# Performance work log

Hardware: AMD Instinct MI355X
Metric: run time of the kernel (lower is better)

Reference implementation:

```python
import jax, jax.numpy as jnp
import numpy as np

N_EMBD = 768
N_HEAD = 8
HEAD_DIM = N_EMBD // N_HEAD


def setup_inputs() -> dict:
    key = jax.random.key(0)
    k1, k2, k3, k4, k5 = jax.random.split(key, 5)
    B, T, C = 8, 1024, N_EMBD
    scale = 0.02
    return {
        "x": jax.random.normal(k1, (B, T, C), dtype=jnp.float32),
        "W_attn": jax.random.normal(k2, (C, 3 * C), dtype=jnp.float32) * scale,
        "b_attn": jnp.zeros((3 * C,), dtype=jnp.float32),
        "W_proj": jax.random.normal(k3, (C, C), dtype=jnp.float32) * scale,
        "b_proj": jnp.zeros((C,), dtype=jnp.float32),
    }


def reference(x, W_attn, b_attn, W_proj, b_proj):
    B, T, C = x.shape
    H, D = N_HEAD, HEAD_DIM
    qkv = x @ W_attn + b_attn                      # [B,T,3C]
    q, k, v = jnp.split(qkv, 3, axis=-1)
    # [B,H,T,D]
    q = q.reshape(B, T, H, D).transpose(0, 2, 1, 3)
    k = k.reshape(B, T, H, D).transpose(0, 2, 1, 3)
    v = v.reshape(B, T, H, D).transpose(0, 2, 1, 3)
    att = jnp.einsum("bhqd,bhkd->bhqk", q, k) * (1.0 / jnp.sqrt(jnp.float32(D)))
    causal = jnp.tril(jnp.ones((T, T), dtype=bool))
    att = jnp.where(causal[None, None], att, jnp.float32(-jnp.inf))
    att = jax.nn.softmax(att, axis=-1)
    y = jnp.einsum("bhqk,bhkd->bhqd", att, v)      # [B,H,T,D]
    y = y.transpose(0, 2, 1, 3).reshape(B, T, C)
    return y @ W_proj + b_proj
```

## Files before the change

kernel.cpp:

```cpp
#include <hip/hip_runtime.h>
#include <math.h>

#define B_ 8
#define T_ 1024
#define C_ 768
#define H_ 8
#define D_ 96
#define M_ (B_ * T_)
#define N1_ (3 * C_)
#define KD_ 768
#define QS_ 1536

typedef __bf16 bf16x8 __attribute__((ext_vector_type(8)));
typedef float f32x4 __attribute__((ext_vector_type(4)));
typedef float f32x16 __attribute__((ext_vector_type(16)));

__device__ __forceinline__ unsigned short f2bf(float f) {
  unsigned int u = __float_as_uint(f);
  u += 0x7FFF + ((u >> 16) & 1);
  return (unsigned short)(u >> 16);
}

__device__ __forceinline__ void load_lds16(const void* g, void* l) {
  __builtin_amdgcn_global_load_lds(
      (const __attribute__((address_space(1))) unsigned int*)g,
      (__attribute__((address_space(3))) unsigned int*)l, 16, 0, 0);
}

__global__ __launch_bounds__(256) void prep_kernel(
    const float* __restrict__ x, unsigned short* __restrict__ xb,
    const float* __restrict__ Wa, unsigned short* __restrict__ WaT,
    const float* __restrict__ Wp, unsigned short* __restrict__ WpT) {
  __shared__ float Lt[32][33];
  int bid = blockIdx.x;
  if (bid < 6144) {
    int i = (bid * 256 + threadIdx.x) * 4;
    float4 v = *(const float4*)(x + i);
    ushort4 o;
    o.x = f2bf(v.x); o.y = f2bf(v.y); o.z = f2bf(v.z); o.w = f2bf(v.w);
    *(ushort4*)(xb + i) = o;
    return;
  }
  bid -= 6144;
  const float* W; unsigned short* WT; int Nd;
  if (bid < 1728) { W = Wa; WT = WaT; Nd = N1_; }
  else            { W = Wp; WT = WpT; Nd = C_; bid -= 1728; }
  const int r0 = (bid % 24) * 32;
  const int c0 = (bid / 24) * 32;
#pragma unroll
  for (int i = 0; i < 4; ++i) {
    int e = threadIdx.x + 256 * i;
    int r = e >> 5, c = e & 31;
    Lt[r][c] = W[(size_t)(r0 + r) * Nd + c0 + c];
  }
  __syncthreads();
#pragma unroll
  for (int i = 0; i < 4; ++i) {
    int e = threadIdx.x + 256 * i;
    int rr = e >> 5, cc = e & 31;
    WT[(size_t)(c0 + rr) * KD_ + r0 + cc] = f2bf(Lt[cc][rr]);
  }
}

template <bool OUTF32, bool VSCAT>
__global__ __launch_bounds__(256, 4) void gemm_mfma_kernel(
    const unsigned short* __restrict__ A, const unsigned short* __restrict__ Bt,
    const float* __restrict__ bias, void* __restrict__ Cout,
    unsigned short* __restrict__ vt, int N,
    int sc_lim, float sc, int mmask, int mshift) {
  constexpr int NCH = 16;
  constexpr int CPW = 4;
  __shared__ __align__(16) unsigned short Sb[2][NCH * 512];
  const int tid = threadIdx.x;
  const int w = tid >> 6, l = tid & 63;
  const int l31 = l & 31, lh = l >> 5;
  const int bid = blockIdx.x;
  const int m0 = (bid & mmask) * 128, n0 = (bid >> mshift) * 128;
  const int wrb = (w >> 1) * 2;
  const int wnb = (w & 1) * 2;

  f32x16 acc[2][2];
#pragma unroll
  for (int i = 0; i < 2; ++i)
#pragma unroll
    for (int j = 0; j < 2; ++j)
#pragma unroll
      for (int r = 0; r < 16; ++r) acc[i][j][r] = 0.f;

  const unsigned short* gp[CPW];
#pragma unroll
  for (int i = 0; i < CPW; ++i) {
    const int c = w * CPW + i;
    const int rr = (c & 7) * 16 + (l >> 2);
    const int ck = 8 * ((l & 3) ^ ((l >> 4) & 3));
    gp[i] = (c < 8) ? A  + (size_t)(m0 + rr) * KD_ + ck
                    : Bt + (size_t)(n0 + rr) * KD_ + ck;
  }

#pragma unroll
  for (int i = 0; i < CPW; ++i) {
    load_lds16(gp[i], &Sb[0][(w * CPW + i) * 512]);
    gp[i] += 32;
  }
  asm volatile("s_waitcnt vmcnt(0)" ::: "memory");
  __builtin_amdgcn_s_barrier();
  asm volatile("" ::: "memory");

  const int rhi = l31 >> 4;
  const int rlo = (l31 & 15) * 32;
  const int rx  = (l31 >> 2) & 3;

  int cur = 0;
  for (int k0 = 0; k0 < KD_; k0 += 32) {
    const bool more = (k0 + 32 < KD_);
    if (more) {
#pragma unroll
      for (int i = 0; i < CPW; ++i) {
        load_lds16(gp[i], &Sb[cur ^ 1][(w * CPW + i) * 512]);
        gp[i] += 32;
      }
    }

#pragma unroll
    for (int kh = 0; kh < 2; ++kh) {
      const int q = 2 * kh + lh;
      bf16x8 af[2], bfr[2];
#pragma unroll
      for (int mi = 0; mi < 2; ++mi)
        af[mi] = *(const bf16x8*)
            &Sb[cur][((wrb + mi) * 2 + rhi) * 512 + rlo + ((q ^ rx)) * 8];
#pragma unroll
      for (int ni = 0; ni < 2; ++ni)
        bfr[ni] = *(const bf16x8*)
            &Sb[cur][(8 + (wnb + ni) * 2 + rhi) * 512 + rlo + ((q ^ rx)) * 8];
#pragma unroll
      for (int mi = 0; mi < 2; ++mi)
#pragma unroll
        for (int ni = 0; ni < 2; ++ni)
          acc[mi][ni] = __builtin_amdgcn_mfma_f32_32x32x16_bf16(
              af[mi], bfr[ni], acc[mi][ni], 0, 0, 0);
    }

    if (more) {
      asm volatile("s_waitcnt vmcnt(0)" ::: "memory");
      asm volatile("" ::: "memory");
      __builtin_amdgcn_s_barrier();
      asm volatile("" ::: "memory");
    }
    cur ^= 1;
  }

  const bool vblock = VSCAT && (n0 >= 1536);
#pragma unroll
  for (int mi = 0; mi < 2; ++mi) {
    const int rowb = m0 + (wrb + mi) * 32 + 4 * lh;
#pragma unroll
    for (int ni = 0; ni < 2; ++ni) {
      const int col = n0 + (wnb + ni) * 32 + l31;
      const float bv = bias[col];
      if (!vblock) {
        const float mul = (col < sc_lim) ? sc : 1.f;
#pragma unroll
        for (int r = 0; r < 16; ++r) {
          const int row = rowb + (r & 3) + 8 * (r >> 2);
          float v = (acc[mi][ni][r] + bv) * mul;
          if (OUTF32)
            ((float*)Cout)[(size_t)row * N + col] = v;
          else
            ((unsigned short*)Cout)[(size_t)row * N + col] = f2bf(v);
        }
      } else {
        const int x = col - 1536;
        const int h = x / 96, d = x % 96;
#pragma unroll
        for (int r = 0; r < 16; ++r) {
          const int row = rowb + (r & 3) + 8 * (r >> 2);
          const int bb = row >> 10, t = row & 1023;
          vt[((size_t)(bb * H_ + h) * D_ + d) * T_ + t] =
              f2bf(acc[mi][ni][r] + bv);
        }
      }
    }
  }
}

__global__ __launch_bounds__(256) void attn_mfma_kernel(
    const unsigned short* __restrict__ qkv,
    const unsigned short* __restrict__ vt,
    unsigned short* __restrict__ y) {
  __shared__ __align__(16) unsigned short KV[2][24 * 512];
  __shared__ __align__(16) unsigned short Pt[4][16][72];

  const int tid = threadIdx.x;
  const int w = tid >> 6, l = tid & 63;
  const int lm = l & 15, lq = l >> 4;
  const int bh = blockIdx.x & 63, pi = blockIdx.x >> 6;
  const int b = bh >> 3, h = bh & 7;
  const size_t bT = (size_t)b * T_;

  bf16x8 onef;
#pragma unroll
  for (int i = 0; i < 8; ++i) onef[i] = (__bf16)1.0f;

  auto issue = [&](int j0, int buf) {
#pragma unroll
    for (int i = 0; i < 6; ++i) {
      const int c = w * 6 + i;
      const unsigned short* g;
      if (c < 12) {
        const int kc = c >> 2, nb = c & 3;
        g = qkv + (bT + j0 + nb * 16 + lm) * QS_ + C_ + h * D_ + kc * 32 + lq * 8;
      } else {
        const int cv = c - 12;
        const int db = cv >> 1, vc = cv & 1;
        g = vt + ((size_t)bh * D_ + db * 16 + lm) * T_ + j0 + vc * 32 + lq * 8;
      }
      load_lds16(g, &KV[buf][c * 512]);
    }
  };

  int cur = 0;
  issue(0, 0);

  for (int half = 0; half < 2; ++half) {
    const int qt = half ? (15 - pi) : pi;
    const int q0 = qt * 64;

    bf16x8 qf[3];
    {
      const unsigned short* qp =
          qkv + (bT + q0 + w * 16 + lm) * QS_ + h * D_ + lq * 8;
      qf[0] = *(const bf16x8*)(qp);
      qf[1] = *(const bf16x8*)(qp + 32);
      qf[2] = *(const bf16x8*)(qp + 64);
    }
    f32x4 o[7];
#pragma unroll
    for (int i = 0; i < 7; ++i) o[i] = (f32x4){0.f, 0.f, 0.f, 0.f};

    for (int jt = 0; jt <= qt; ++jt) {
      __syncthreads();
      if (jt < qt)          issue((jt + 1) * 64, cur ^ 1);
      else if (half == 0)   issue(0, cur ^ 1);

      const bool diag = (jt == qt);
#pragma unroll
      for (int nb = 0; nb < 4; ++nb) {
        if (diag && nb > w) {
#pragma unroll
          for (int r = 0; r < 4; ++r)
            Pt[w][lq * 4 + r][nb * 16 + lm] = 0;
          continue;
        }
        f32x4 a = (f32x4){0.f, 0.f, 0.f, 0.f};
#pragma unroll
        for (int kc = 0; kc < 3; ++kc) {
          bf16x8 kf = *(const bf16x8*)&KV[cur][(kc * 4 + nb) * 512 + l * 8];
          a = __builtin_amdgcn_mfma_f32_16x16x32_bf16(qf[kc], kf, a, 0, 0, 0);
        }
#pragma unroll
        for (int r = 0; r < 4; ++r) {
          float s = a[r];
          if (diag && (nb * 16 + lm > w * 16 + lq * 4 + r)) s = -INFINITY;
          Pt[w][lq * 4 + r][nb * 16 + lm] = f2bf(__expf(s));
        }
      }

      bf16x8 pf0 = *(const bf16x8*)&Pt[w][lm][lq * 8];
      bf16x8 pf1 = *(const bf16x8*)&Pt[w][lm][32 + lq * 8];
#pragma unroll
      for (int db = 0; db < 6; ++db) {
        bf16x8 vf0 = *(const bf16x8*)&KV[cur][(12 + db * 2 + 0) * 512 + l * 8];
        bf16x8 vf1 = *(const bf16x8*)&KV[cur][(12 + db * 2 + 1) * 512 + l * 8];
        o[db] = __builtin_amdgcn_mfma_f32_16x16x32_bf16(pf0, vf0, o[db], 0, 0, 0);
        o[db] = __builtin_amdgcn_mfma_f32_16x16x32_bf16(pf1, vf1, o[db], 0, 0, 0);
      }
      o[6] = __builtin_amdgcn_mfma_f32_16x16x32_bf16(pf0, onef, o[6], 0, 0, 0);
      o[6] = __builtin_amdgcn_mfma_f32_16x16x32_bf16(pf1, onef, o[6], 0, 0, 0);
      cur ^= 1;
    }

#pragma unroll
    for (int r = 0; r < 4; ++r) {
      const float inv = 1.f / o[6][r];
      const size_t row = bT + q0 + w * 16 + lq * 4 + r;
#pragma unroll
      for (int db = 0; db < 6; ++db)
        y[row * C_ + h * D_ + db * 16 + lm] = f2bf(o[db][r] * inv);
    }
  }
}

extern "C" void kernel_launch(void* const* d_in, const int* in_sizes, int n_in,
                              void* d_out, int out_size, void* d_ws, size_t ws_size,
                              hipStream_t stream) {
  const float* x      = (const float*)d_in[0];
  const float* W_attn = (const float*)d_in[1];
  const float* b_attn = (const float*)d_in[2];
  const float* W_proj = (const float*)d_in[3];
  const float* b_proj = (const float*)d_in[4];
  float* out = (float*)d_out;

  char* ws = (char*)d_ws;
  unsigned short* xb  = (unsigned short*)(ws);
  unsigned short* WaT = (unsigned short*)(ws + 12582912);
  unsigned short* WpT = (unsigned short*)(ws + 16121856);
  unsigned short* qkv = (unsigned short*)(ws + 17301504);
  unsigned short* vt  = (unsigned short*)(ws + 42467328);
  unsigned short* yb  = xb;

  const float qscale = 0.10206207261596577f;

  prep_kernel<<<6144 + 2304, 256, 0, stream>>>(x, xb, W_attn, WaT, W_proj, WpT);

  gemm_mfma_kernel<false, true><<<(N1_ / 128) * (M_ / 128), 256, 0, stream>>>(
      xb, WaT, b_attn, qkv, vt, QS_, C_, qscale, 63, 6);
  attn_mfma_kernel<<<8 * B_ * H_, 256, 0, stream>>>(qkv, vt, yb);
  gemm_mfma_kernel<true, false><<<(C_ / 128) * (M_ / 128), 256, 0, stream>>>(
      yb, WpT, b_proj, out, nullptr, C_, 0, 1.f, 63, 6);
}
```

Baseline: 184.6 us.

## Process two 64-row query sub-tiles per attention block to reuse K/V tiles

Each attention block now handles 128 query rows (two 64-row sub-tiles per wave) instead of 64, sharing every K/V tile loaded into LDS across both sub-tiles. This halves K/V global loads and synchronisations per query, and the causal mask handles the two diagonal tiles per sub-tile. The grid shrinks to half as many blocks and per-thread accumulator registers double, which reduces parallelism and may lower occupancy.

Result: no change. 187.7 us (+1.7%).

```diff
diff --git a/kernel.cpp b/kernel.cpp
--- a/kernel.cpp
+++ b/kernel.cpp
@@ -189,12 +189,12 @@
     const unsigned short* __restrict__ vt,
     unsigned short* __restrict__ y) {
   __shared__ __align__(16) unsigned short KV[2][24 * 512];
-  __shared__ __align__(16) unsigned short Pt[4][16][72];
+  __shared__ __align__(16) unsigned short Pt[2][4][16][72];
 
   const int tid = threadIdx.x;
   const int w = tid >> 6, l = tid & 63;
   const int lm = l & 15, lq = l >> 4;
-  const int bh = blockIdx.x & 63, pi = blockIdx.x >> 6;
+  const int bh = blockIdx.x & 63, pj = blockIdx.x >> 6;
   const int b = bh >> 3, h = bh & 7;
   const size_t bT = (size_t)b * T_;
 
@@ -223,71 +223,94 @@
   issue(0, 0);
 
   for (int half = 0; half < 2; ++half) {
-    const int qt = half ? (15 - pi) : pi;
-    const int q0 = qt * 64;
-
-    bf16x8 qf[3];
-    {
+    const int qt = half ? (7 - pj) : pj;
+    const int q0 = qt * 128;
+    const int nt = 2 * qt + 2;
+
+    bf16x8 qf[2][3];
+#pragma unroll
+    for (int s = 0; s < 2; ++s) {
       const unsigned short* qp =
-          qkv + (bT + q0 + w * 16 + lm) * QS_ + h * D_ + lq * 8;
-      qf[0] = *(const bf16x8*)(qp);
-      qf[1] = *(const bf16x8*)(qp + 32);
-      qf[2] = *(const bf16x8*)(qp + 64);
-    }
-    f32x4 o[7];
-#pragma unroll
-    for (int i = 0; i < 7; ++i) o[i] = (f32x4){0.f, 0.f, 0.f, 0.f};
-
-    for (int jt = 0; jt <= qt; ++jt) {
+          qkv + (bT + q0 + s * 64 + w * 16 + lm) * QS_ + h * D_ + lq * 8;
+      qf[s][0] = *(const bf16x8*)(qp);
+      qf[s][1] = *(const bf16x8*)(qp + 32);
+      qf[s][2] = *(const bf16x8*)(qp + 64);
+    }
+    f32x4 o[2][7];
+#pragma unroll
+    for (int s = 0; s < 2; ++s)
+#pragma unroll
+      for (int i = 0; i < 7; ++i) o[s][i] = (f32x4){0.f, 0.f, 0.f, 0.f};
+
+    for (int jt = 0; jt < nt; ++jt) {
       __syncthreads();
-      if (jt < qt)          issue((jt + 1) * 64, cur ^ 1);
-      else if (half == 0)   issue(0, cur ^ 1);
-
-      const bool diag = (jt == qt);
+      if (jt + 1 < nt)     issue((jt + 1) * 64, cur ^ 1);
+      else if (half == 0)  issue(0, cur ^ 1);
+
+      const int d0 = (jt == 2 * qt) ? 1 : ((jt == 2 * qt + 1) ? 2 : 0);
+      const int d1 = (jt == 2 * qt + 1) ? 1 : 0;
+
 #pragma unroll
       for (int nb = 0; nb < 4; ++nb) {
-        if (diag && nb > w) {
-#pragma unroll
-          for (int r = 0; r < 4; ++r)
-            Pt[w][lq * 4 + r][nb * 16 + lm] = 0;
-          continue;
+        bf16x8 kf0 = *(const bf16x8*)&KV[cur][(0 * 4 + nb) * 512 + l * 8];
+        bf16x8 kf1 = *(const bf16x8*)&KV[cur][(1 * 4 + nb) * 512 + l * 8];
+        bf16x8 kf2 = *(const bf16x8*)&KV[cur][(2 * 4 + nb) * 512 + l * 8];
+#pragma unroll
+        for (int s = 0; s < 2; ++s) {
+          const int ds = s ? d1 : d0;
+          if (ds == 2 || (ds == 1 && nb > w)) {
+#pragma unroll
+            for (int r = 0; r < 4; ++r)
+              Pt[s][w][lq * 4 + r][nb * 16 + lm] = 0;
+            continue;
+          }
+          f32x4 a = (f32x4){0.f, 0.f, 0.f, 0.f};
+          a = __builtin_amdgcn_mfma_f32_16x16x32_bf16(qf[s][0], kf0, a, 0, 0, 0);
+          a = __builtin_amdgcn_mfma_f32_16x16x32_bf16(qf[s][1], kf1, a, 0, 0, 0);
+          a = __builtin_amdgcn_mfma_f32_16x16x32_bf16(qf[s][2], kf2, a, 0, 0, 0);
+#pragma unroll
+          for (int r = 0; r < 4; ++r) {
+            float sv = a[r];
+            if (ds == 1 && (nb * 16 + lm > w * 16 + lq * 4 + r)) sv = -INFINITY;
+            Pt[s][w][lq * 4 + r][nb * 16 + lm] = f2bf(__expf(sv));
+          }
         }
-        f32x4 a = (f32x4){0.f, 0.f, 0.f, 0.f};
-#pragma unroll
-        for (int kc = 0; kc < 3; ++kc) {
-          bf16x8 kf = *(const bf16x8*)&KV[cur][(kc * 4 + nb) * 512 + l * 8];
-          a = __builtin_amdgcn_mfma_f32_16x16x32_bf16(qf[kc], kf, a, 0, 0, 0);
-        }
-#pragma unroll
-        for (int r = 0; r < 4; ++r) {
-          float s = a[r];
-          if (diag && (nb * 16 + lm > w * 16 + lq * 4 + r)) s = -INFINITY;
-          Pt[w][lq * 4 + r][nb * 16 + lm] = f2bf(__expf(s));
-        }
-      }
-
-      bf16x8 pf0 = *(const bf16x8*)&Pt[w][lm][lq * 8];
-      bf16x8 pf1 = *(const bf16x8*)&Pt[w][lm][32 + lq * 8];
+      }
+
+      bf16x8 pf[2][2];
+#pragma unroll
+      for (int s = 0; s < 2; ++s) {
+        pf[s][0] = *(const bf16x8*)&Pt[s][w][lm][lq * 8];
+        pf[s][1] = *(const bf16x8*)&Pt[s][w][lm][32 + lq * 8];
+      }
 #pragma unroll
       for (int db = 0; db < 6; ++db) {
         bf16x8 vf0 = *(const bf16x8*)&KV[cur][(12 + db * 2 + 0) * 512 + l * 8];
         bf16x8 vf1 = *(const bf16x8*)&KV[cur][(12 + db * 2 + 1) * 512 + l * 8];
-        o[db] = __builtin_amdgcn_mfma_f32_16x16x32_bf16(pf0, vf0, o[db], 0, 0, 0);
-        o[db] = __builtin_amdgcn_mfma_f32_16x16x32_bf16(pf1, vf1, o[db], 0, 0, 0);
-      }
-      o[6] = __builtin_amdgcn_mfma_f32_16x16x32_bf16(pf0, onef, o[6], 0, 0, 0);
-      o[6] = __builtin_amdgcn_mfma_f32_16x16x32_bf16(pf1, onef, o[6], 0, 0, 0);
+#pragma unroll
+        for (int s = 0; s < 2; ++s) {
+          o[s][db] = __builtin_amdgcn_mfma_f32_16x16x32_bf16(pf[s][0], vf0, o[s][db], 0, 0, 0);
+          o[s][db] = __builtin_amdgcn_mfma_f32_16x16x32_bf16(pf[s][1], vf1, o[s][db], 0, 0, 0);
+        }
+      }
+#pragma unroll
+      for (int s = 0; s < 2; ++s) {
+        o[s][6] = __builtin_amdgcn_mfma_f32_16x16x32_bf16(pf[s][0], onef, o[s][6], 0, 0, 0);
+        o[s][6] = __builtin_amdgcn_mfma_f32_16x16x32_bf16(pf[s][1], onef, o[s][6], 0, 0, 0);
+      }
       cur ^= 1;
     }
 
 #pragma unroll
-    for (int r = 0; r < 4; ++r) {
-      const float inv = 1.f / o[6][r];
-      const size_t row = bT + q0 + w * 16 + lq * 4 + r;
-#pragma unroll
-      for (int db = 0; db < 6; ++db)
-        y[row * C_ + h * D_ + db * 16 + lm] = f2bf(o[db][r] * inv);
-    }
+    for (int s = 0; s < 2; ++s)
+#pragma unroll
+      for (int r = 0; r < 4; ++r) {
+        const float inv = 1.f / o[s][6][r];
+        const size_t row = bT + q0 + s * 64 + w * 16 + lq * 4 + r;
+#pragma unroll
+        for (int db = 0; db < 6; ++db)
+          y[row * C_ + h * D_ + db * 16 + lm] = f2bf(o[s][db][r] * inv);
+      }
   }
 }
 
@@ -315,7 +338,7 @@
 
   gemm_mfma_kernel<false, true><<<(N1_ / 128) * (M_ / 128), 256, 0, stream>>>(
       xb, WaT, b_attn, qkv, vt, QS_, C_, qscale, 63, 6);
-  attn_mfma_kernel<<<8 * B_ * H_, 256, 0, stream>>>(qkv, vt, yb);
+  attn_mfma_kernel<<<4 * B_ * H_, 256, 0, stream>>>(qkv, vt, yb);
   gemm_mfma_kernel<true, false><<<(C_ / 128) * (M_ / 128), 256, 0, stream>>>(
       yb, WpT, b_proj, out, nullptr, C_, 0, 1.f, 63, 6);
 }
```
